# Kernel optimization log

Measured on AMD Instinct MI355X. Metric: run time of the kernel, lower is better.

The kernel has to match this reference:

```python
import jax, jax.numpy as jnp
import numpy as np

B, S, HOPS, DIM, NREL = 1024, 32, 2, 64, 237
NENT, NEDGE = 14541, 272115
SIGMA = 0.1
CFMW = 64


def setup_inputs() -> dict:
    key = jax.random.key(0)
    ks = jax.random.split(key, 20)

    def g(k, shape):
        return (jax.random.normal(k, shape, dtype=jnp.float32) / np.float32(np.sqrt(shape[0])))

    inp = {
        "entity_pairs": jax.random.randint(ks[0], (B, 2), 0, NENT),
        "train_edges": jax.random.randint(ks[1], (B,), 0, NEDGE),
        "labels": jax.random.randint(ks[2], (B,), 0, NREL),
        "entity2edges": jax.random.randint(ks[3], (NENT + 1, S), 0, NEDGE + 1),
        "edge2entities": jax.random.randint(ks[4], (NEDGE + 1, 1), 0, NENT + 1),
        "edge2relation": jax.random.randint(ks[5], (NEDGE + 1,), 0, NREL + 1),
        "t": jax.random.uniform(ks[6], (B,), dtype=jnp.float32),
        "eps": jax.random.normal(ks[7], (B, NREL), dtype=jnp.float32),
        "rel_feat": g(ks[8], (NREL, DIM)),
        "W_agg0": g(ks[9], (DIM, DIM)), "b_agg0": jnp.zeros((DIM,), jnp.float32),
        "W_agg1": g(ks[10], (DIM, NREL)), "b_agg1": jnp.zeros((NREL,), jnp.float32),
        "W_out": g(ks[11], (2 * NREL, NREL)), "b_out": jnp.zeros((NREL,), jnp.float32),
        "mW1": g(ks[12], (NREL + 1, CFMW)), "mb1": jnp.zeros((CFMW,), jnp.float32),
        "mW2": g(ks[13], (CFMW, CFMW)), "mb2": jnp.zeros((CFMW,), jnp.float32),
        "mW3": g(ks[14], (CFMW, CFMW)), "mb3": jnp.zeros((CFMW,), jnp.float32),
        "mW4": g(ks[15], (CFMW, NREL)), "mb4": jnp.zeros((NREL,), jnp.float32),
    }
    return inp


def _side(ent, labels, train_edges, entity2edges, edge2entities, edge2relation, relf, aggs):
    # multi-hop neighbor edge gather + masks (exclude the training edge itself)
    edges_list = [labels]  # hop-0 "edges" are the relation labels
    masks = []
    for i in range(HOPS):
        if i == 0:
            ne = ent.reshape(B, 1)  # (B, 1) source entities
        else:
            ne = edge2entities[edges_list[-1].reshape(-1)].reshape(B, -1)
        nedges = entity2edges[ne.reshape(-1)].reshape(B, -1)  # (B, S**(i+1))
        edges_list.append(nedges)
        masks.append((nedges != train_edges[:, None]).astype(relf.dtype))
    # edge -> relation -> feature
    ev = [relf[edges_list[0]]]  # (B, DIM)
    for edges in edges_list[1:]:
        ev.append(relf[edge2relation[edges]])  # (B, S**h, DIM)
    # iterative mean aggregation (PathCon-style, one entity per edge)
    for i in range(HOPS):
        W, b, act, self_inc = aggs[i]
        d = W.shape[0]
        nxt = []
        for hop in range(HOPS - i):
            neigh = ev[hop + 1].reshape(B, -1, 1, S, d)
            m = masks[hop].reshape(B, -1, 1, S, 1)
            out = jnp.mean(jnp.mean(neigh * m, axis=-2), axis=-2)  # (B, S**hop, d)
            if self_inc:
                out = out + ev[hop].reshape(B, -1, d)
            nxt.append(act(out @ W + b))
        ev = nxt
    return ev[0].reshape(B, NREL)


def reference(entity_pairs, train_edges, labels, entity2edges, edge2entities,
              edge2relation, t, eps, rel_feat, W_agg0, b_agg0, W_agg1, b_agg1,
              W_out, b_out, mW1, mb1, mW2, mb2, mW3, mb3, mW4, mb4):
    relf = jnp.concatenate([rel_feat, jnp.zeros((1, DIM), rel_feat.dtype)], axis=0)
    aggs = [
        (W_agg0, b_agg0, jax.nn.relu, True),    # intermediate hop: relu, self-included
        (W_agg1, b_agg1, lambda x: x, False),   # last hop: identity, no self
    ]
    x0 = _side(entity_pairs[:, 0], labels, train_edges, entity2edges,
               edge2entities, edge2relation, relf, aggs)
    x1 = _side(entity_pairs[:, 1], labels, train_edges, entity2edges,
               edge2entities, edge2relation, relf, aggs)
    output = jnp.concatenate([x0, x1], axis=-1) @ W_out + b_out  # (B, NREL)
    # CFM: xt = (1-t) x0 + t x1 + sigma*eps ; ut = x1 - x0
    tb = t[:, None]
    xt = (1.0 - tb) * x0 + tb * x1 + SIGMA * eps
    h = jnp.concatenate([xt, tb], axis=-1)
    h = jax.nn.selu(h @ mW1 + mb1)
    h = jax.nn.selu(h @ mW2 + mb2)
    h = jax.nn.selu(h @ mW3 + mb3)
    vt = h @ mW4 + mb4
    scores = output * vt
    return scores
```

## Files before the change

### kernel.cpp

```cpp
#include <hip/hip_runtime.h>
#include <math.h>

#define BB 1024
#define S 32
#define DIM 64
#define NREL 237
#define SIGMA 0.1f

#define OFS_WR    0
#define N_WR      (238*64)
#define OFS_WC0   (OFS_WR + N_WR)
#define N_WC      (64*237)
#define OFS_WC1   (OFS_WC0 + N_WC)
#define OFS_BC    (OFS_WC1 + N_WC)
#define OFS_HC    (OFS_BC + 237)

#define LDS_BYTES 71936

__device__ __forceinline__ float selu_f(float x) {
    const float alpha = 1.6732632423543772f;
    const float scale = 1.0507009873554805f;
    return scale * (x > 0.f ? x : alpha * expm1f(x));
}

__global__ __launch_bounds__(256) void precompute_kernel(
    const float* __restrict__ rel_feat, const float* __restrict__ W0,
    const float* __restrict__ W1, const float* __restrict__ b1,
    const float* __restrict__ W_out, const float* __restrict__ b_out,
    const float* __restrict__ mW1, const float* __restrict__ mb1,
    float* __restrict__ ws) {
    __shared__ float red[256];
    int blk = blockIdx.x;
    const int tid = threadIdx.x;

    if (blk < 60) {
        int idx = blk * 256 + tid;
        if (idx < 238 * 64) {
            int r = idx >> 6, o = idx & 63;
            float acc = 0.f;
            if (r < NREL) {
#pragma unroll 8
                for (int d = 0; d < 64; ++d)
                    acc += rel_feat[r * 64 + d] * W0[d * 64 + o];
            }
            ws[OFS_WR + idx] = acc;
        }
        return;
    }
    blk -= 60;
    if (blk < 512) {
        int half = blk >> 8;
        int lb = blk & 255;
        int o = lb >> 2, ct = lb & 3;
        int cl = tid & 63, g = tid >> 6;
        int c = ct * 64 + cl;
        const float* Wsrc = W_out + half * 237 * 237;
        float acc = 0.f;
        if (c < NREL) {
            int k0 = g * 60, k1 = (g == 3) ? 237 : (k0 + 60);
#pragma unroll 4
            for (int k = k0; k < k1; ++k)
                acc += W1[o * 237 + k] * Wsrc[k * 237 + c];
        }
        red[tid] = acc;
        __syncthreads();
        if (g == 0 && c < NREL) {
            float s = red[cl] + red[64 + cl] + red[128 + cl] + red[192 + cl];
            ws[(half ? OFS_WC1 : OFS_WC0) + o * 237 + c] = s;
        }
        return;
    }
    blk -= 512;
    if (blk < 4) {
        int cl = tid & 63, g = tid >> 6;
        int c = blk * 64 + cl;
        float acc = 0.f;
        if (c < NREL) {
            int k0 = g * 60, k1 = (g == 3) ? 237 : (k0 + 60);
#pragma unroll 4
            for (int k = k0; k < k1; ++k)
                acc += b1[k] * (W_out[k * 237 + c] + W_out[(237 + k) * 237 + c]);
        }
        red[tid] = acc;
        __syncthreads();
        if (g == 0 && c < NREL)
            ws[OFS_BC + c] = b_out[c] + red[cl] + red[64 + cl] + red[128 + cl] + red[192 + cl];
        return;
    }
    {
        int w = tid & 63, g = tid >> 6;
        int k0 = g * 60, k1 = (g == 3) ? 237 : (k0 + 60);
        float acc = 0.f;
#pragma unroll 4
        for (int k = k0; k < k1; ++k)
            acc += b1[k] * mW1[k * 64 + w];
        red[tid] = acc;
        __syncthreads();
        if (g == 0)
            ws[OFS_HC + w] = mb1[w] + red[w] + red[64 + w] + red[128 + w] + red[192 + w];
    }
}

__global__ __launch_bounds__(256, 2) void gf_kernel(
    const int* __restrict__ ep, const int* __restrict__ te_arr,
    const int* __restrict__ e2e_tab, const int* __restrict__ e2ent,
    const int* __restrict__ e2r, const float* __restrict__ b0,
    const float* __restrict__ t_arr, const float* __restrict__ eps,
    const float* __restrict__ W1, const float* __restrict__ mW1,
    const float* __restrict__ mW2, const float* __restrict__ mb2,
    const float* __restrict__ mW3, const float* __restrict__ mb3,
    const float* __restrict__ mW4, const float* __restrict__ mb4,
    const float* __restrict__ ws, float* __restrict__ out) {
    extern __shared__ float smem[];
    float* s_wr      = smem;
    int*   s_r2m     = (int*)(smem + 15232);
    int*   s_r1      = (int*)(smem + 16256);
    int*   s_ent2    = (int*)(smem + 16384);
    float* s_m1      = smem + 16512;
    float* s_partial = smem + 16640;
    float* s_ov      = smem + 17728;

    const int tid = threadIdx.x;
    const int bb = blockIdx.x * 2;
    const int g = tid >> 4;
    const int c = tid & 15;
    const int te0 = te_arr[bb];
    const int te1 = te_arr[bb + 1];
    const float4 b0v = ((const float4*)b0)[c];

    {
        const float4* src = (const float4*)(ws + OFS_WR);
        float4* dst = (float4*)s_wr;
        for (int i = tid; i < 238 * 16; i += 256) dst[i] = src[i];
    }
    const float4* sWr4 = (const float4*)s_wr;

    if (tid < 128) {
        int u = tid >> 5, s = tid & 31;
        int b = bb + (u >> 1), side = u & 1;
        int te = (u >> 1) ? te1 : te0;
        int ent = ep[b * 2 + side];
        int e1 = e2e_tab[ent * S + s];
        s_r1[u * 32 + s] = e2r[e1];
        s_m1[u * 32 + s] = (e1 != te) ? 1.0f : 0.0f;
        s_ent2[u * 32 + s] = e2ent[e1];
    }
    __syncthreads();

    {
        const int te = te0;
        for (int p = tid; p < 1024; p += 256) {
            int j = p >> 5, s = p & 31;
            int e2 = e2e_tab[s_ent2[j] * S + s];
            s_r2m[p] = (e2 == te) ? NREL : e2r[e2];
        }
    }
    __syncthreads();

    for (int u = 0; u < 4; ++u) {
        const int jA = g, jB = g + 16;
        const int* rrA = &s_r2m[jA * 32];
        const int* rrB = &s_r2m[jB * 32];
        float4 aA = sWr4[s_r1[u * 32 + jA] * 16 + c];
        float4 aB = sWr4[s_r1[u * 32 + jB] * 16 + c];
        float4 sA = make_float4(0.f, 0.f, 0.f, 0.f);
        float4 sB = make_float4(0.f, 0.f, 0.f, 0.f);
#pragma unroll
        for (int s = 0; s < 32; ++s) {
            float4 vA = sWr4[rrA[s] * 16 + c];
            float4 vB = sWr4[rrB[s] * 16 + c];
            sA.x += vA.x; sA.y += vA.y; sA.z += vA.z; sA.w += vA.w;
            sB.x += vB.x; sB.y += vB.y; sB.z += vB.z; sB.w += vB.w;
        }
        const float inv = 1.0f / 32.0f;
        float mA = s_m1[u * 32 + jA];
        float mB = s_m1[u * 32 + jB];
        float4 r;
        r.x = fmaxf(aA.x + sA.x * inv + b0v.x, 0.f) * mA
            + fmaxf(aB.x + sB.x * inv + b0v.x, 0.f) * mB;
        r.y = fmaxf(aA.y + sA.y * inv + b0v.y, 0.f) * mA
            + fmaxf(aB.y + sB.y * inv + b0v.y, 0.f) * mB;
        r.z = fmaxf(aA.z + sA.z * inv + b0v.z, 0.f) * mA
            + fmaxf(aB.z + sB.z * inv + b0v.z, 0.f) * mB;
        r.w = fmaxf(aA.w + sA.w * inv + b0v.w, 0.f) * mA
            + fmaxf(aB.w + sB.w * inv + b0v.w, 0.f) * mB;
        *((float4*)&s_partial[g * 68 + c * 4]) = r;
        __syncthreads();
        if (tid < 64) {
            float sum = 0.f;
#pragma unroll
            for (int j = 0; j < 16; ++j) sum += s_partial[j * 68 + tid];
            s_ov[u * 64 + tid] = sum * (1.0f / 32.0f);
        }
        if (u < 3) {
            const int un = u + 1;
            const int te = (un >> 1) ? te1 : te0;
            for (int p = tid; p < 1024; p += 256) {
                int j = p >> 5, s = p & 31;
                int e2 = e2e_tab[s_ent2[un * 32 + j] * S + s];
                s_r2m[p] = (e2 == te) ? NREL : e2r[e2];
            }
        }
        __syncthreads();
    }

    float* s_omix = smem;
    float* s_ymix = smem + 128;
    float* s_out  = smem + 608;
    float* s_red  = smem + 1088;
    float* s_h    = smem + 1600;
    const float tb0v = t_arr[bb];
    const float tb1v = t_arr[bb + 1];
    const float* Wc0 = ws + OFS_WC0;
    const float* Wc1 = ws + OFS_WC1;
    const float* bc = ws + OFS_BC;
    const float* hc = ws + OFS_HC;

    if (tid < 128) {
        int p = tid >> 6, w = tid & 63;
        float tb = p ? tb1v : tb0v;
        float o0 = s_ov[(p * 2 + 0) * 64 + w];
        float o1 = s_ov[(p * 2 + 1) * 64 + w];
        s_omix[p * 64 + w] = (1.f - tb) * o0 + tb * o1;
    }
    __syncthreads();

    if (tid < NREL) {
        float y0 = 0.f, y1 = 0.f;
#pragma unroll 4
        for (int d = 0; d < 64; ++d) {
            float w1v = W1[d * 237 + tid];
            y0 += s_omix[d] * w1v;
            y1 += s_omix[64 + d] * w1v;
        }
        s_ymix[tid] = y0;
        s_ymix[240 + tid] = y1;
        float a0 = bc[tid], a1 = a0;
#pragma unroll 4
        for (int d = 0; d < 64; ++d) {
            float w0 = Wc0[d * 237 + tid];
            float w1 = Wc1[d * 237 + tid];
            a0 += s_ov[d] * w0 + s_ov[64 + d] * w1;
            a1 += s_ov[128 + d] * w0 + s_ov[192 + d] * w1;
        }
        s_out[tid] = a0;
        s_out[240 + tid] = a1;
    }
    __syncthreads();

    {
        int w = tid & 63, gg = tid >> 6;
        float a0 = 0.f, a1 = 0.f;
        int k0 = gg * 60, k1 = (gg == 3) ? 237 : (k0 + 60);
        const float* e0 = eps + bb * 237;
        const float* e1 = eps + (bb + 1) * 237;
#pragma unroll 4
        for (int k = k0; k < k1; ++k) {
            float m = mW1[k * 64 + w];
            a0 += (SIGMA * e0[k] + s_ymix[k]) * m;
            a1 += (SIGMA * e1[k] + s_ymix[240 + k]) * m;
        }
        s_red[tid] = a0;
        s_red[256 + tid] = a1;
    }
    __syncthreads();
    if (tid < 128) {
        int p = tid >> 6, w = tid & 63;
        float tb = p ? tb1v : tb0v;
        float h = hc[w] + tb * mW1[237 * 64 + w]
                + s_red[p * 256 + w] + s_red[p * 256 + 64 + w]
                + s_red[p * 256 + 128 + w] + s_red[p * 256 + 192 + w];
        s_h[p * 64 + w] = selu_f(h);
    }
    __syncthreads();

    {
        int w = tid & 63, gg = tid >> 6;
        float a0 = 0.f, a1 = 0.f;
#pragma unroll
        for (int d = gg * 16; d < gg * 16 + 16; ++d) {
            float m = mW2[d * 64 + w];
            a0 += s_h[d] * m;
            a1 += s_h[64 + d] * m;
        }
        s_red[tid] = a0;
        s_red[256 + tid] = a1;
    }
    __syncthreads();
    if (tid < 128) {
        int p = tid >> 6, w = tid & 63;
        float v = mb2[w] + s_red[p * 256 + w] + s_red[p * 256 + 64 + w]
                + s_red[p * 256 + 128 + w] + s_red[p * 256 + 192 + w];
        s_h[p * 64 + w] = selu_f(v);
    }
    __syncthreads();

    {
        int w = tid & 63, gg = tid >> 6;
        float a0 = 0.f, a1 = 0.f;
#pragma unroll
        for (int d = gg * 16; d < gg * 16 + 16; ++d) {
            float m = mW3[d * 64 + w];
            a0 += s_h[d] * m;
            a1 += s_h[64 + d] * m;
        }
        s_red[tid] = a0;
        s_red[256 + tid] = a1;
    }
    __syncthreads();
    if (tid < 128) {
        int p = tid >> 6, w = tid & 63;
        float v = mb3[w] + s_red[p * 256 + w] + s_red[p * 256 + 64 + w]
                + s_red[p * 256 + 128 + w] + s_red[p * 256 + 192 + w];
        s_h[p * 64 + w] = selu_f(v);
    }
    __syncthreads();

    if (tid < NREL) {
        float a0 = mb4[tid], a1 = a0;
#pragma unroll 4
        for (int w = 0; w < 64; ++w) {
            float m = mW4[w * 237 + tid];
            a0 += s_h[w] * m;
            a1 += s_h[64 + w] * m;
        }
        out[bb * 237 + tid] = s_out[tid] * a0;
        out[(bb + 1) * 237 + tid] = s_out[240 + tid] * a1;
    }
}

extern "C" void kernel_launch(void* const* d_in, const int* in_sizes, int n_in,
                              void* d_out, int out_size, void* d_ws, size_t ws_size,
                              hipStream_t stream) {
    const int* ep       = (const int*)d_in[0];
    const int* te       = (const int*)d_in[1];
    const int* e2e      = (const int*)d_in[3];
    const int* e2ent    = (const int*)d_in[4];
    const int* e2r      = (const int*)d_in[5];
    const float* t      = (const float*)d_in[6];
    const float* eps    = (const float*)d_in[7];
    const float* relf   = (const float*)d_in[8];
    const float* W0     = (const float*)d_in[9];
    const float* b0     = (const float*)d_in[10];
    const float* W1     = (const float*)d_in[11];
    const float* b1     = (const float*)d_in[12];
    const float* W_out  = (const float*)d_in[13];
    const float* b_out  = (const float*)d_in[14];
    const float* mW1    = (const float*)d_in[15];
    const float* mb1    = (const float*)d_in[16];
    const float* mW2    = (const float*)d_in[17];
    const float* mb2    = (const float*)d_in[18];
    const float* mW3    = (const float*)d_in[19];
    const float* mb3    = (const float*)d_in[20];
    const float* mW4    = (const float*)d_in[21];
    const float* mb4    = (const float*)d_in[22];
    float* ws  = (float*)d_ws;
    float* out = (float*)d_out;

    hipLaunchKernelGGL(precompute_kernel, dim3(577), dim3(256), 0, stream,
                       relf, W0, W1, b1, W_out, b_out, mW1, mb1, ws);
    hipLaunchKernelGGL(gf_kernel, dim3(BB / 2), dim3(256), LDS_BYTES, stream,
                       ep, te, e2e, e2ent, e2r, b0,
                       t, eps, W1, mW1, mW2, mb2, mW3, mb3, mW4, mb4, ws, out);
}
```

Measured before the change: 157.4 us.

## Drop W1·W_out precompute, pack hop-2 indices as bytes, use wave-shuffle reductions

The precompute kernel now only builds rel_feat·W0; the folded W1·W_out matrices and folded biases are gone, so the main kernel computes x = ov·W1 + b1 per side and then a full 237x474 W_out product per pair, plus explicit xt for the CFM input. Hop-2 relation indices are stored as bytes in LDS and all four units are gathered up front, which removes the per-unit barriers. Partial sums are reduced with wave shuffles, and launch_bounds drops the min-2-blocks hint. The goal is less precompute work and fewer syncs and LDS bytes, at the cost of many more FLOPs per block in the output projection.

```diff
diff --git a/kernel.cpp b/kernel.cpp
--- a/kernel.cpp
+++ b/kernel.cpp
@@ -8,14 +8,8 @@
 #define SIGMA 0.1f
 
 #define OFS_WR    0
-#define N_WR      (238*64)
-#define OFS_WC0   (OFS_WR + N_WR)
-#define N_WC      (64*237)
-#define OFS_WC1   (OFS_WC0 + N_WC)
-#define OFS_BC    (OFS_WC1 + N_WC)
-#define OFS_HC    (OFS_BC + 237)
-
-#define LDS_BYTES 71936
+
+#define LDS_BYTES 71296
 
 __device__ __forceinline__ float selu_f(float x) {
     const float alpha = 1.6732632423543772f;
@@ -23,102 +17,45 @@
     return scale * (x > 0.f ? x : alpha * expm1f(x));
 }
 
-__global__ __launch_bounds__(256) void precompute_kernel(
+__global__ __launch_bounds__(256) void pre_wr_kernel(
     const float* __restrict__ rel_feat, const float* __restrict__ W0,
-    const float* __restrict__ W1, const float* __restrict__ b1,
-    const float* __restrict__ W_out, const float* __restrict__ b_out,
-    const float* __restrict__ mW1, const float* __restrict__ mb1,
     float* __restrict__ ws) {
     __shared__ float red[256];
-    int blk = blockIdx.x;
+    const int r = blockIdx.x;
     const int tid = threadIdx.x;
-
-    if (blk < 60) {
-        int idx = blk * 256 + tid;
-        if (idx < 238 * 64) {
-            int r = idx >> 6, o = idx & 63;
-            float acc = 0.f;
-            if (r < NREL) {
-#pragma unroll 8
-                for (int d = 0; d < 64; ++d)
-                    acc += rel_feat[r * 64 + d] * W0[d * 64 + o];
-            }
-            ws[OFS_WR + idx] = acc;
-        }
-        return;
-    }
-    blk -= 60;
-    if (blk < 512) {
-        int half = blk >> 8;
-        int lb = blk & 255;
-        int o = lb >> 2, ct = lb & 3;
-        int cl = tid & 63, g = tid >> 6;
-        int c = ct * 64 + cl;
-        const float* Wsrc = W_out + half * 237 * 237;
-        float acc = 0.f;
-        if (c < NREL) {
-            int k0 = g * 60, k1 = (g == 3) ? 237 : (k0 + 60);
-#pragma unroll 4
-            for (int k = k0; k < k1; ++k)
-                acc += W1[o * 237 + k] * Wsrc[k * 237 + c];
-        }
-        red[tid] = acc;
-        __syncthreads();
-        if (g == 0 && c < NREL) {
-            float s = red[cl] + red[64 + cl] + red[128 + cl] + red[192 + cl];
-            ws[(half ? OFS_WC1 : OFS_WC0) + o * 237 + c] = s;
-        }
-        return;
-    }
-    blk -= 512;
-    if (blk < 4) {
-        int cl = tid & 63, g = tid >> 6;
-        int c = blk * 64 + cl;
-        float acc = 0.f;
-        if (c < NREL) {
-            int k0 = g * 60, k1 = (g == 3) ? 237 : (k0 + 60);
-#pragma unroll 4
-            for (int k = k0; k < k1; ++k)
-                acc += b1[k] * (W_out[k * 237 + c] + W_out[(237 + k) * 237 + c]);
-        }
-        red[tid] = acc;
-        __syncthreads();
-        if (g == 0 && c < NREL)
-            ws[OFS_BC + c] = b_out[c] + red[cl] + red[64 + cl] + red[128 + cl] + red[192 + cl];
-        return;
-    }
-    {
-        int w = tid & 63, g = tid >> 6;
-        int k0 = g * 60, k1 = (g == 3) ? 237 : (k0 + 60);
-        float acc = 0.f;
-#pragma unroll 4
-        for (int k = k0; k < k1; ++k)
-            acc += b1[k] * mW1[k * 64 + w];
-        red[tid] = acc;
-        __syncthreads();
-        if (g == 0)
-            ws[OFS_HC + w] = mb1[w] + red[w] + red[64 + w] + red[128 + w] + red[192 + w];
-    }
-}
-
-__global__ __launch_bounds__(256, 2) void gf_kernel(
+    const int o = tid & 63, q = tid >> 6;
+    float acc = 0.f;
+    if (r < NREL) {
+#pragma unroll
+        for (int d = q * 16; d < q * 16 + 16; ++d)
+            acc += rel_feat[r * 64 + d] * W0[d * 64 + o];
+    }
+    red[tid] = acc;
+    __syncthreads();
+    if (q == 0)
+        ws[OFS_WR + r * 64 + o] = red[o] + red[64 + o] + red[128 + o] + red[192 + o];
+}
+
+__global__ __launch_bounds__(256) void gf_kernel(
     const int* __restrict__ ep, const int* __restrict__ te_arr,
     const int* __restrict__ e2e_tab, const int* __restrict__ e2ent,
     const int* __restrict__ e2r, const float* __restrict__ b0,
     const float* __restrict__ t_arr, const float* __restrict__ eps,
-    const float* __restrict__ W1, const float* __restrict__ mW1,
+    const float* __restrict__ W1, const float* __restrict__ b1,
+    const float* __restrict__ W_out, const float* __restrict__ b_out,
+    const float* __restrict__ mW1, const float* __restrict__ mb1,
     const float* __restrict__ mW2, const float* __restrict__ mb2,
     const float* __restrict__ mW3, const float* __restrict__ mb3,
     const float* __restrict__ mW4, const float* __restrict__ mb4,
     const float* __restrict__ ws, float* __restrict__ out) {
     extern __shared__ float smem[];
-    float* s_wr      = smem;
-    int*   s_r2m     = (int*)(smem + 15232);
-    int*   s_r1      = (int*)(smem + 16256);
-    int*   s_ent2    = (int*)(smem + 16384);
-    float* s_m1      = smem + 16512;
-    float* s_partial = smem + 16640;
-    float* s_ov      = smem + 17728;
+    float*         s_wr   = smem;
+    unsigned char* s_r2m8 = (unsigned char*)(smem + 15232);
+    unsigned char* s_r1u  = (unsigned char*)(smem + 16256);
+    float*         s_m1   = smem + 16288;
+    int*           s_ent2 = (int*)(smem + 16416);
+    float*         s_wp   = smem + 16544;
+    float*         s_ov   = smem + 17568;
 
     const int tid = threadIdx.x;
     const int bb = blockIdx.x * 2;
@@ -141,38 +78,49 @@
         int te = (u >> 1) ? te1 : te0;
         int ent = ep[b * 2 + side];
         int e1 = e2e_tab[ent * S + s];
-        s_r1[u * 32 + s] = e2r[e1];
+        s_r1u[u * 32 + s] = (unsigned char)e2r[e1];
         s_m1[u * 32 + s] = (e1 != te) ? 1.0f : 0.0f;
         s_ent2[u * 32 + s] = e2ent[e1];
     }
     __syncthreads();
 
-    {
-        const int te = te0;
-        for (int p = tid; p < 1024; p += 256) {
-            int j = p >> 5, s = p & 31;
-            int e2 = e2e_tab[s_ent2[j] * S + s];
-            s_r2m[p] = (e2 == te) ? NREL : e2r[e2];
-        }
-    }
-    __syncthreads();
-
+    for (int p = tid; p < 4096; p += 256) {
+        int u = p >> 10, q = p & 1023, j = q >> 5, s2 = q & 31;
+        int te = (u >> 1) ? te1 : te0;
+        int e2 = e2e_tab[s_ent2[u * 32 + j] * S + s2];
+        s_r2m8[p] = (unsigned char)((e2 == te) ? NREL : e2r[e2]);
+    }
+    __syncthreads();
+
+    const float inv = 1.0f / 32.0f;
     for (int u = 0; u < 4; ++u) {
         const int jA = g, jB = g + 16;
-        const int* rrA = &s_r2m[jA * 32];
-        const int* rrB = &s_r2m[jB * 32];
-        float4 aA = sWr4[s_r1[u * 32 + jA] * 16 + c];
-        float4 aB = sWr4[s_r1[u * 32 + jB] * 16 + c];
+        float4 aA = sWr4[(int)s_r1u[u * 32 + jA] * 16 + c];
+        float4 aB = sWr4[(int)s_r1u[u * 32 + jB] * 16 + c];
+        const uint4* pA = (const uint4*)(s_r2m8 + u * 1024 + jA * 32);
+        const uint4* pB = (const uint4*)(s_r2m8 + u * 1024 + jB * 32);
+        uint4 iA0 = pA[0], iA1 = pA[1];
+        uint4 iB0 = pB[0], iB1 = pB[1];
         float4 sA = make_float4(0.f, 0.f, 0.f, 0.f);
         float4 sB = make_float4(0.f, 0.f, 0.f, 0.f);
-#pragma unroll
-        for (int s = 0; s < 32; ++s) {
-            float4 vA = sWr4[rrA[s] * 16 + c];
-            float4 vB = sWr4[rrB[s] * 16 + c];
-            sA.x += vA.x; sA.y += vA.y; sA.z += vA.z; sA.w += vA.w;
-            sB.x += vB.x; sB.y += vB.y; sB.z += vB.z; sB.w += vB.w;
-        }
-        const float inv = 1.0f / 32.0f;
+#define ACC4(sum, word) { unsigned int wv = (word);                       \
+        float4 v0 = sWr4[(wv & 255u) * 16 + c];                           \
+        float4 v1 = sWr4[((wv >> 8) & 255u) * 16 + c];                    \
+        float4 v2 = sWr4[((wv >> 16) & 255u) * 16 + c];                   \
+        float4 v3 = sWr4[(wv >> 24) * 16 + c];                            \
+        sum.x += (v0.x + v1.x) + (v2.x + v3.x);                           \
+        sum.y += (v0.y + v1.y) + (v2.y + v3.y);                           \
+        sum.z += (v0.z + v1.z) + (v2.z + v3.z);                           \
+        sum.w += (v0.w + v1.w) + (v2.w + v3.w); }
+        ACC4(sA, iA0.x) ACC4(sB, iB0.x)
+        ACC4(sA, iA0.y) ACC4(sB, iB0.y)
+        ACC4(sA, iA0.z) ACC4(sB, iB0.z)
+        ACC4(sA, iA0.w) ACC4(sB, iB0.w)
+        ACC4(sA, iA1.x) ACC4(sB, iB1.x)
+        ACC4(sA, iA1.y) ACC4(sB, iB1.y)
+        ACC4(sA, iA1.z) ACC4(sB, iB1.z)
+        ACC4(sA, iA1.w) ACC4(sB, iB1.w)
+#undef ACC4
         float mA = s_m1[u * 32 + jA];
         float mB = s_m1[u * 32 + jB];
         float4 r;
@@ -184,67 +132,58 @@
             + fmaxf(aB.z + sB.z * inv + b0v.z, 0.f) * mB;
         r.w = fmaxf(aA.w + sA.w * inv + b0v.w, 0.f) * mA
             + fmaxf(aB.w + sB.w * inv + b0v.w, 0.f) * mB;
-        *((float4*)&s_partial[g * 68 + c * 4]) = r;
-        __syncthreads();
-        if (tid < 64) {
-            float sum = 0.f;
-#pragma unroll
-            for (int j = 0; j < 16; ++j) sum += s_partial[j * 68 + tid];
-            s_ov[u * 64 + tid] = sum * (1.0f / 32.0f);
-        }
-        if (u < 3) {
-            const int un = u + 1;
-            const int te = (un >> 1) ? te1 : te0;
-            for (int p = tid; p < 1024; p += 256) {
-                int j = p >> 5, s = p & 31;
-                int e2 = e2e_tab[s_ent2[un * 32 + j] * S + s];
-                s_r2m[p] = (e2 == te) ? NREL : e2r[e2];
-            }
-        }
-        __syncthreads();
-    }
-
-    float* s_omix = smem;
-    float* s_ymix = smem + 128;
-    float* s_out  = smem + 608;
-    float* s_red  = smem + 1088;
-    float* s_h    = smem + 1600;
+        r.x += __shfl_xor(r.x, 16); r.x += __shfl_xor(r.x, 32);
+        r.y += __shfl_xor(r.y, 16); r.y += __shfl_xor(r.y, 32);
+        r.z += __shfl_xor(r.z, 16); r.z += __shfl_xor(r.z, 32);
+        r.w += __shfl_xor(r.w, 16); r.w += __shfl_xor(r.w, 32);
+        if ((tid & 63) < 16)
+            ((float4*)s_wp)[(u * 4 + (tid >> 6)) * 16 + c] = r;
+    }
+    __syncthreads();
+    {
+        int u = tid >> 6, w = tid & 63;
+        int base = (u * 4 * 16 + (w >> 2)) * 4 + (w & 3);
+        float s = s_wp[base] + s_wp[base + 64] + s_wp[base + 128] + s_wp[base + 192];
+        s_ov[u * 64 + w] = s * inv;
+    }
+    __syncthreads();
+
+    float* s_x   = smem;
+    float* s_xt  = smem + 960;
+    float* s_out = smem + 1440;
+    float* s_red = smem + 1920;
+    float* s_h   = smem + 2432;
     const float tb0v = t_arr[bb];
     const float tb1v = t_arr[bb + 1];
-    const float* Wc0 = ws + OFS_WC0;
-    const float* Wc1 = ws + OFS_WC1;
-    const float* bc = ws + OFS_BC;
-    const float* hc = ws + OFS_HC;
-
-    if (tid < 128) {
-        int p = tid >> 6, w = tid & 63;
-        float tb = p ? tb1v : tb0v;
-        float o0 = s_ov[(p * 2 + 0) * 64 + w];
-        float o1 = s_ov[(p * 2 + 1) * 64 + w];
-        s_omix[p * 64 + w] = (1.f - tb) * o0 + tb * o1;
-    }
-    __syncthreads();
 
     if (tid < NREL) {
-        float y0 = 0.f, y1 = 0.f;
+        float y0 = 0.f, y1 = 0.f, y2 = 0.f, y3 = 0.f;
 #pragma unroll 4
         for (int d = 0; d < 64; ++d) {
             float w1v = W1[d * 237 + tid];
-            y0 += s_omix[d] * w1v;
-            y1 += s_omix[64 + d] * w1v;
-        }
-        s_ymix[tid] = y0;
-        s_ymix[240 + tid] = y1;
-        float a0 = bc[tid], a1 = a0;
-#pragma unroll 4
-        for (int d = 0; d < 64; ++d) {
-            float w0 = Wc0[d * 237 + tid];
-            float w1 = Wc1[d * 237 + tid];
-            a0 += s_ov[d] * w0 + s_ov[64 + d] * w1;
-            a1 += s_ov[128 + d] * w0 + s_ov[192 + d] * w1;
-        }
-        s_out[tid] = a0;
-        s_out[240 + tid] = a1;
+            y0 += s_ov[d] * w1v;       y1 += s_ov[64 + d] * w1v;
+            y2 += s_ov[128 + d] * w1v; y3 += s_ov[192 + d] * w1v;
+        }
+        float bv = b1[tid];
+        s_x[tid] = y0 + bv;       s_x[240 + tid] = y1 + bv;
+        s_x[480 + tid] = y2 + bv; s_x[720 + tid] = y3 + bv;
+    }
+    __syncthreads();
+
+    if (tid < NREL) {
+        s_xt[tid]       = (1.f - tb0v) * s_x[tid] + tb0v * s_x[240 + tid]
+                        + SIGMA * eps[bb * 237 + tid];
+        s_xt[240 + tid] = (1.f - tb1v) * s_x[480 + tid] + tb1v * s_x[720 + tid]
+                        + SIGMA * eps[(bb + 1) * 237 + tid];
+        float a0 = b_out[tid], a1 = a0;
+#pragma unroll 2
+        for (int k = 0; k < NREL; ++k) {
+            float wt = W_out[k * 237 + tid];
+            float wb = W_out[(237 + k) * 237 + tid];
+            a0 += s_x[k] * wt + s_x[240 + k] * wb;
+            a1 += s_x[480 + k] * wt + s_x[720 + k] * wb;
+        }
+        s_out[tid] = a0; s_out[240 + tid] = a1;
     }
     __syncthreads();
 
@@ -252,22 +191,19 @@
         int w = tid & 63, gg = tid >> 6;
         float a0 = 0.f, a1 = 0.f;
         int k0 = gg * 60, k1 = (gg == 3) ? 237 : (k0 + 60);
-        const float* e0 = eps + bb * 237;
-        const float* e1 = eps + (bb + 1) * 237;
 #pragma unroll 4
         for (int k = k0; k < k1; ++k) {
             float m = mW1[k * 64 + w];
-            a0 += (SIGMA * e0[k] + s_ymix[k]) * m;
-            a1 += (SIGMA * e1[k] + s_ymix[240 + k]) * m;
-        }
-        s_red[tid] = a0;
-        s_red[256 + tid] = a1;
+            a0 += s_xt[k] * m;
+            a1 += s_xt[240 + k] * m;
+        }
+        s_red[tid] = a0; s_red[256 + tid] = a1;
     }
     __syncthreads();
     if (tid < 128) {
         int p = tid >> 6, w = tid & 63;
         float tb = p ? tb1v : tb0v;
-        float h = hc[w] + tb * mW1[237 * 64 + w]
+        float h = mb1[w] + tb * mW1[237 * 64 + w]
                 + s_red[p * 256 + w] + s_red[p * 256 + 64 + w]
                 + s_red[p * 256 + 128 + w] + s_red[p * 256 + 192 + w];
         s_h[p * 64 + w] = selu_f(h);
@@ -280,11 +216,9 @@
 #pragma unroll
         for (int d = gg * 16; d < gg * 16 + 16; ++d) {
             float m = mW2[d * 64 + w];
-            a0 += s_h[d] * m;
-            a1 += s_h[64 + d] * m;
-        }
-        s_red[tid] = a0;
-        s_red[256 + tid] = a1;
+            a0 += s_h[d] * m; a1 += s_h[64 + d] * m;
+        }
+        s_red[tid] = a0; s_red[256 + tid] = a1;
     }
     __syncthreads();
     if (tid < 128) {
@@ -301,11 +235,9 @@
 #pragma unroll
         for (int d = gg * 16; d < gg * 16 + 16; ++d) {
             float m = mW3[d * 64 + w];
-            a0 += s_h[d] * m;
-            a1 += s_h[64 + d] * m;
-        }
-        s_red[tid] = a0;
-        s_red[256 + tid] = a1;
+            a0 += s_h[d] * m; a1 += s_h[64 + d] * m;
+        }
+        s_red[tid] = a0; s_red[256 + tid] = a1;
     }
     __syncthreads();
     if (tid < 128) {
@@ -321,8 +253,7 @@
 #pragma unroll 4
         for (int w = 0; w < 64; ++w) {
             float m = mW4[w * 237 + tid];
-            a0 += s_h[w] * m;
-            a1 += s_h[64 + w] * m;
+            a0 += s_h[w] * m; a1 += s_h[64 + w] * m;
         }
         out[bb * 237 + tid] = s_out[tid] * a0;
         out[(bb + 1) * 237 + tid] = s_out[240 + tid] * a1;
@@ -357,9 +288,10 @@
     float* ws  = (float*)d_ws;
     float* out = (float*)d_out;
 
-    hipLaunchKernelGGL(precompute_kernel, dim3(577), dim3(256), 0, stream,
-                       relf, W0, W1, b1, W_out, b_out, mW1, mb1, ws);
+    hipLaunchKernelGGL(pre_wr_kernel, dim3(238), dim3(256), 0, stream,
+                       relf, W0, ws);
     hipLaunchKernelGGL(gf_kernel, dim3(BB / 2), dim3(256), LDS_BYTES, stream,
                        ep, te, e2e, e2ent, e2r, b0,
-                       t, eps, W1, mW1, mW2, mb2, mW3, mb3, mW4, mb4, ws, out);
-}
+                       t, eps, W1, b1, W_out, b_out,
+                       mW1, mb1, mW2, mb2, mW3, mb3, mW4, mb4, ws, out);
+}
```

Measured after the change: 211.4 us. +34.3%, slower.
